# Kernel tuning notes

Measured on AMD Instinct MI355X. Metric: run time of the kernel, lower is better.

Reference implementation:

```python
import jax, jax.numpy as jnp
import numpy as np

B, L, H = 64, 512, 512  # batch_size, input_size (src len), hidden_size


def setup_inputs() -> dict:
    key = jax.random.key(0)
    ks = jax.random.split(key, 12)
    return {
        "encoder_outputs": jax.random.normal(ks[0], (B, L, H), dtype=jnp.float32),
        "attn_mask": jax.random.randint(ks[1], (B, L), 0, 2, dtype=jnp.int64),
        "hidden": jax.random.normal(ks[2], (B, H), dtype=jnp.float32),
        "coverage": jax.random.uniform(ks[3], (B, L), dtype=jnp.float32),
        # attnLin: Linear(H, H)
        "attn_w": jax.random.normal(ks[4], (H, H), dtype=jnp.float32) * 0.02,
        "attn_b": jax.random.normal(ks[5], (H,), dtype=jnp.float32) * 0.02,
        # decoderAttnLinear: Linear(H, H)
        "dec_w": jax.random.normal(ks[6], (H, H), dtype=jnp.float32) * 0.02,
        "dec_b": jax.random.normal(ks[7], (H,), dtype=jnp.float32) * 0.02,
        # cvgConv: Conv2d(L, L, kernel=(1, H), padding='same') -> weight [L, L, 1, H]
        "cvg_w": jax.random.normal(ks[8], (L, L, 1, H), dtype=jnp.float32) * 0.02,
        "cvg_b": jax.random.normal(ks[9], (L,), dtype=jnp.float32) * 0.02,
        # v parameter (trunc_normal in torch; plain normal is fine as a baseline)
        "v": jax.random.normal(ks[10], (B, H), dtype=jnp.float32),
    }


def reference(encoder_outputs, attn_mask, hidden, coverage,
              attn_w, attn_b, dec_w, dec_b, cvg_w, cvg_b, v):
    # Per-position linear loop in torch == one batched linear over [B, L, H].
    enc_feat = jnp.einsum('blh,oh->blo', encoder_outputs, attn_w) + attn_b  # [B,L,H]
    dec_feat = (hidden @ dec_w.T + dec_b)[:, None, :]                        # [B,1,H]
    # Coverage conv: input is [B, L(channels), 1, 1]; kernel (1, H) with 'same'
    # padding means only kernel column kw = (H-1)//2 ever overlaps the single
    # real (non-zero-padded) pixel, so the conv reduces exactly to a matmul
    # with that weight column plus bias. Same math, no wasted zero-multiplies.
    center = (H - 1) // 2
    w_eff = cvg_w[:, :, 0, center]                                           # [L_out, L_in]
    cov_feat = (coverage @ w_eff.T + cvg_b)[:, :, None]                      # [B,L,1]
    feats = jnp.tanh(enc_feat + dec_feat + cov_feat)                         # [B,L,H]
    scores = jnp.einsum('blh,bh->bl', feats, v)                              # [B,L]
    scores = jnp.where(attn_mask == 1, scores, -jnp.inf)
    attn_weights = jax.nn.softmax(scores, axis=1)                            # [B,L]
    new_coverage = coverage + attn_weights                                   # coverage += aw
    context_vector = jnp.einsum('bl,blh->bh', attn_weights, encoder_outputs) # [B,H]
    return context_vector, attn_weights, new_coverage
```

## Files before the change

kernel.cpp:

```cpp
#include <hip/hip_runtime.h>

#define B_ 64
#define L_ 512
#define H_ 512
#define CENTER 255

typedef float  f32x4  __attribute__((ext_vector_type(4)));
typedef _Float16 f16x8 __attribute__((ext_vector_type(8)));
typedef unsigned short u16x4 __attribute__((ext_vector_type(4)));
typedef unsigned short USH;


__device__ __forceinline__ float fast_tanh(float x) {
    float e = __expf(2.0f * x);
    return 1.0f - 2.0f * __builtin_amdgcn_rcpf(e + 1.0f);
}

__launch_bounds__(512)
__global__ void pre_kernel(const float* __restrict__ cvg_w, const float* __restrict__ cvg_b,
                           const float* __restrict__ coverage,
                           const float* __restrict__ aw, USH* __restrict__ bh16,
                           const float* __restrict__ hidden, const float* __restrict__ dec_w,
                           const float* __restrict__ dec_b,
                           float* __restrict__ dec_feat, float* __restrict__ cov_feat) {
    __shared__ float pool[34304];
    const int bid = blockIdx.x, t = threadIdx.x;
    if (bid < 512) {
        float* wl = pool;
        float* cs = pool + 512;
        const int i = bid;
        wl[t] = cvg_w[((size_t)(i * L_ + t)) * H_ + CENTER];
        #pragma unroll 8
        for (int c = 0; c < 64; ++c)
            cs[t * 65 + c] = coverage[c * L_ + t];
        __syncthreads();
        const int b = t >> 3, jg = t & 7;
        float sum = 0.f;
        #pragma unroll 8
        for (int jj = 0; jj < 64; ++jj) {
            int j = jg * 64 + ((jj + jg * 8) & 63);
            sum += cs[j * 65 + b] * wl[j];
        }
        sum += __shfl_xor(sum, 1, 64);
        sum += __shfl_xor(sum, 2, 64);
        sum += __shfl_xor(sum, 4, 64);
        if (jg == 0) cov_feat[b * L_ + i] = sum + cvg_b[i];
    } else if (bid < 640) {
        int i = (bid - 512) * 512 + t;
        float4 x = *(const float4*)&aw[(size_t)i * 4];
        float xs[4] = {x.x, x.y, x.z, x.w};
        u16x4 h;
        #pragma unroll
        for (int j = 0; j < 4; ++j)
            h[j] = __builtin_bit_cast(USH, (_Float16)xs[j]);
        *(u16x4*)&bh16[(size_t)i * 4] = h;
    } else {
        float* sbuf = pool;
        float* pr   = pool + 512;
        const int blk = bid - 640, b = blk >> 2, qq = blk & 3;
        const int ol = t & 127, part = t >> 7;
        sbuf[t] = hidden[b * H_ + t];
        __syncthreads();
        const float* row  = dec_w + (size_t)(qq * 128 + ol) * H_ + part * 128;
        const float* hseg = sbuf + part * 128;
        float d0 = 0.f, d1 = 0.f, d2 = 0.f, d3 = 0.f;
        #pragma unroll
        for (int k = 0; k < 128; k += 16) {
            float4 w0 = *(const float4*)&row[k];
            float4 w1 = *(const float4*)&row[k + 4];
            float4 w2 = *(const float4*)&row[k + 8];
            float4 w3 = *(const float4*)&row[k + 12];
            d0 += w0.x * hseg[k]      + w0.y * hseg[k + 1]  + w0.z * hseg[k + 2]  + w0.w * hseg[k + 3];
            d1 += w1.x * hseg[k + 4]  + w1.y * hseg[k + 5]  + w1.z * hseg[k + 6]  + w1.w * hseg[k + 7];
            d2 += w2.x * hseg[k + 8]  + w2.y * hseg[k + 9]  + w2.z * hseg[k + 10] + w2.w * hseg[k + 11];
            d3 += w3.x * hseg[k + 12] + w3.y * hseg[k + 13] + w3.z * hseg[k + 14] + w3.w * hseg[k + 15];
        }
        pr[t] = d0 + d1 + d2 + d3;
        __syncthreads();
        if (t < 128)
            dec_feat[b * H_ + qq * 128 + t] = pr[t] + pr[t + 128] + pr[t + 256] + pr[t + 384]
                                              + dec_b[qq * 128 + t];
    }
}

#define BM 128

#define STAGE_B(BUF, KS1)                                                                  \
    {                                                                                      \
        _Pragma("unroll")                                                                  \
        for (int it = 0; it < 2; ++it)                                                     \
            __builtin_amdgcn_global_load_lds(                                              \
                (const __attribute__((address_space(1))) void*)(bh16 + goffB[it] + (KS1) * 32), \
                (__attribute__((address_space(3))) void*)&Bsh[BUF][(wv * 2 + it) * 512],   \
                16, 0, 0);                                                                 \
    }

#define CVTWRITEA(BUF, A4)                                                                 \
    {                                                                                      \
        float axs[4] = {A4.x, A4.y, A4.z, A4.w};                                           \
        u16x4 hh;                                                                          \
        _Pragma("unroll")                                                                  \
        for (int j = 0; j < 4; ++j)                                                        \
            hh[j] = __builtin_bit_cast(USH, (_Float16)axs[j]);                             \
        *(u16x4*)&Ash[BUF][awoff] = hh;                                                    \
    }

__launch_bounds__(1024, 4)
__global__ void fused_score_mfma(const float* __restrict__ enc,
                                 const USH* __restrict__ bh16,
                                 const float* __restrict__ attn_b,
                                 const float* __restrict__ dec_feat,
                                 const float* __restrict__ cov_feat,
                                 const float* __restrict__ v,
                                 float* __restrict__ scores) {
    __shared__ USH Bsh[3][16384];
    __shared__ USH Ash[2][4096];

    const int t  = threadIdx.x;
    const int wv = t >> 6, ln = t & 63;
    const int wr = wv >> 3, wc = wv & 7;
    const int q  = ln >> 4, cl = ln & 15;
    const int m0 = blockIdx.x * BM;
    const int b  = blockIdx.x >> 2;

    int goffB[2];
    #pragma unroll
    for (int it = 0; it < 2; ++it) {
        int c   = wv * 2 + it;
        int srl = ln >> 3;
        int u   = (ln & 7) ^ (srl & 7);
        int n   = c * 16 + srl * 2 + (u >> 2);
        goffB[it] = n * 512 + (u & 3) * 8;
    }
    const int sA   = (((cl & 1) * 4 + q) ^ ((cl >> 1) & 7)) * 8;
    const int aoff = wr * 2048 + (cl >> 1) * 64 + sA;
    const int boff = wc * 2048 + (cl >> 1) * 64 + sA;

    const int arow = t >> 3, akoct = t & 7;
    const int asw  = ((arow & 1) * 4 + (akoct >> 1)) ^ ((arow >> 1) & 7);
    const int awoff = (arow >> 1) * 64 + asw * 8 + (akoct & 1) * 4;
    const float* agsrc = enc + (size_t)(m0 + arow) * H_ + akoct * 4;

    f32x4 acc[4][4];
    #pragma unroll
    for (int mf = 0; mf < 4; ++mf)
        #pragma unroll
        for (int nf = 0; nf < 4; ++nf) acc[mf][nf] = (f32x4){0.f, 0.f, 0.f, 0.f};

    float4 aP = *(const float4*)(agsrc + 32);
    float4 c0 = *(const float4*)agsrc;
    __builtin_amdgcn_sched_barrier(0);
    STAGE_B(0, 0);
    STAGE_B(1, 1);
    __builtin_amdgcn_sched_barrier(0);
    CVTWRITEA(0, c0);
    asm volatile("s_waitcnt lgkmcnt(0)" ::: "memory");
    asm volatile("s_waitcnt vmcnt(2)" ::: "memory");
    __builtin_amdgcn_sched_barrier(0);
    __builtin_amdgcn_s_barrier();

    #pragma unroll
    for (int ks = 0; ks < 16; ++ks) {
        const int curB = ks % 3;
        const int curA = ks & 1, nxtA = curA ^ 1;
        float4 aN;
        if (ks < 14) {
            STAGE_B((ks + 2) % 3, ks + 2);
            aN = *(const float4*)(agsrc + (ks + 2) * 32);
            __builtin_amdgcn_sched_barrier(0);
        }

        f16x8 ah[4];
        #pragma unroll
        for (int mf = 0; mf < 4; ++mf)
            ah[mf] = *(const f16x8*)&Ash[curA][aoff + mf * 512];
        __builtin_amdgcn_s_setprio(1);
        #pragma unroll
        for (int nf = 0; nf < 4; ++nf) {
            f16x8 bh = *(const f16x8*)&Bsh[curB][boff + nf * 512];
            #pragma unroll
            for (int mf = 0; mf < 4; ++mf)
                acc[mf][nf] = __builtin_amdgcn_mfma_f32_16x16x32_f16(ah[mf], bh, acc[mf][nf], 0, 0, 0);
        }
        __builtin_amdgcn_s_setprio(0);

        if (ks < 15) {
            CVTWRITEA(nxtA, aP);
            aP = aN;
            asm volatile("s_waitcnt lgkmcnt(0)" ::: "memory");
            if (ks < 14)
                asm volatile("s_waitcnt vmcnt(3)" ::: "memory");
            else
                asm volatile("s_waitcnt vmcnt(0)" ::: "memory");
            __builtin_amdgcn_sched_barrier(0);
            __builtin_amdgcn_s_barrier();
        }
    }
    __syncthreads();

    float (*scred)[BM] = (float (*)[BM])Ash;
    float addv[4], vvv[4];
    #pragma unroll
    for (int nf = 0; nf < 4; ++nf) {
        int n = wc * 64 + nf * 16 + cl;
        addv[nf] = attn_b[n] + dec_feat[b * H_ + n];
        vvv[nf]  = v[b * H_ + n];
    }
    #pragma unroll
    for (int mf = 0; mf < 4; ++mf) {
        #pragma unroll
        for (int reg = 0; reg < 4; ++reg) {
            int row = wr * 64 + mf * 16 + q * 4 + reg;
            float cf = cov_feat[m0 + row];
            float s = 0.f;
            #pragma unroll
            for (int nf = 0; nf < 4; ++nf)
                s += fast_tanh(acc[mf][nf][reg] + addv[nf] + cf) * vvv[nf];
            s += __shfl_xor(s, 1, 64);
            s += __shfl_xor(s, 2, 64);
            s += __shfl_xor(s, 4, 64);
            s += __shfl_xor(s, 8, 64);
            if (cl == 0) scred[wc][row] = s;
        }
    }
    __syncthreads();
    if (t < BM) {
        float s = 0.f;
        #pragma unroll
        for (int g = 0; g < 8; ++g) s += scred[g][t];
        scores[m0 + t] = s;
    }
}

__launch_bounds__(512)
__global__ void smctx_kernel(const float* __restrict__ scores, const int* __restrict__ mask,
                             const float* __restrict__ coverage, const float* __restrict__ enc,
                             float* __restrict__ out) {
    __shared__ float w[512];
    __shared__ float red[8];
    __shared__ float red2[8];
    __shared__ float cred[4][128];
    const int bid = blockIdx.x, b = bid >> 2, hc = bid & 3, t = threadIdx.x;
    const int idx = b * L_ + t;
    bool m = (mask[idx] == 1);
    float s = scores[idx];
    float val = m ? s : -INFINITY;

    float r = val;
    #pragma unroll
    for (int d = 1; d <= 32; d <<= 1) r = fmaxf(r, __shfl_xor(r, d, 64));
    if ((t & 63) == 0) red[t >> 6] = r;
    __syncthreads();
    float gmax = red[0];
    #pragma unroll
    for (int i = 1; i < 8; ++i) gmax = fmaxf(gmax, red[i]);

    float p = m ? __expf(s - gmax) : 0.f;
    float qq = p;
    #pragma unroll
    for (int d = 1; d <= 32; d <<= 1) qq += __shfl_xor(qq, d, 64);
    if ((t & 63) == 0) red2[t >> 6] = qq;
    __syncthreads();
    float tot = 0.f;
    #pragma unroll
    for (int i = 0; i < 8; ++i) tot += red2[i];

    float wt = p / tot;
    w[t] = wt;
    if (hc == 0) {
        out[B_ * H_ + idx] = wt;
        out[B_ * H_ + B_ * L_ + idx] = coverage[idx] + wt;
    }
    __syncthreads();

    const int ls = t >> 7, hb = t & 127;
    const float* ep = enc + (size_t)b * (L_ * H_) + hc * 128 + hb;
    float a0 = 0.f, a1 = 0.f, a2 = 0.f, a3 = 0.f;
    for (int l = ls; l < L_; l += 16) {
        a0 += w[l]      * ep[(size_t)l * H_];
        a1 += w[l + 4]  * ep[(size_t)(l + 4) * H_];
        a2 += w[l + 8]  * ep[(size_t)(l + 8) * H_];
        a3 += w[l + 12] * ep[(size_t)(l + 12) * H_];
    }
    cred[ls][hb] = a0 + a1 + a2 + a3;
    __syncthreads();
    if (t < 128)
        out[b * H_ + hc * 128 + t] = cred[0][t] + cred[1][t] + cred[2][t] + cred[3][t];
}

extern "C" void kernel_launch(void* const* d_in, const int* in_sizes, int n_in,
                              void* d_out, int out_size, void* d_ws, size_t ws_size,
                              hipStream_t stream) {
    const float* enc      = (const float*)d_in[0];
    const int*   mask     = (const int*)d_in[1];
    const float* hidden   = (const float*)d_in[2];
    const float* coverage = (const float*)d_in[3];
    const float* attn_w   = (const float*)d_in[4];
    const float* attn_b   = (const float*)d_in[5];
    const float* dec_w    = (const float*)d_in[6];
    const float* dec_b    = (const float*)d_in[7];
    const float* cvg_w    = (const float*)d_in[8];
    const float* cvg_b    = (const float*)d_in[9];
    const float* v        = (const float*)d_in[10];
    float* out = (float*)d_out;
    float* ws  = (float*)d_ws;
    float* scores   = ws;
    float* dec_feat = ws + 32768;
    float* cov_feat = ws + 65536;
    USH* bpk = (USH*)(ws + 360448);

    hipLaunchKernelGGL(pre_kernel,       dim3(896),  dim3(512),  0, stream,
                       cvg_w, cvg_b, coverage, attn_w, bpk, hidden, dec_w, dec_b,
                       dec_feat, cov_feat);
    hipLaunchKernelGGL(fused_score_mfma, dim3(256),  dim3(1024), 0, stream,
                       enc, bpk, attn_b, dec_feat, cov_feat, v, scores);
    hipLaunchKernelGGL(smctx_kernel,     dim3(256),  dim3(512),  0, stream,
                       scores, mask, coverage, enc, out);
}
```

Measured before the change: 70.07 us.

## Fuse softmax and context reduction into score kernel via cooperative grid sync

Merges the softmax/context kernel into the MFMA score kernel through a cooperative launch and a grid-wide sync. After the sync, each block recomputes the row softmax and accumulates the context over its own 128-row tile of encoder outputs, which that block just streamed and may still be in cache. Partial context sums are combined with atomicAdd into an output that is zeroed before the sync. This removes one kernel launch and possibly a second pass over the encoder from DRAM. The costs are a grid barrier, redundant softmax work in every block, and float atomics that make the summation order nondeterministic.

Measured after the change: 104.9 us. +49.7%, slower.

```diff
diff --git a/kernel.cpp b/kernel.cpp
--- a/kernel.cpp
+++ b/kernel.cpp
@@ -1,4 +1,7 @@
 #include <hip/hip_runtime.h>
+#include <hip/hip_cooperative_groups.h>
+
+namespace cg = cooperative_groups;
 
 #define B_ 64
 #define L_ 512
@@ -112,7 +115,10 @@
                                  const float* __restrict__ dec_feat,
                                  const float* __restrict__ cov_feat,
                                  const float* __restrict__ v,
-                                 float* __restrict__ scores) {
+                                 float* __restrict__ scores,
+                                 const int* __restrict__ mask,
+                                 const float* __restrict__ coverage,
+                                 float* __restrict__ out) {
     __shared__ USH Bsh[3][16384];
     __shared__ USH Ash[2][4096];
 
@@ -122,6 +128,7 @@
     const int q  = ln >> 4, cl = ln & 15;
     const int m0 = blockIdx.x * BM;
     const int b  = blockIdx.x >> 2;
+    const int lt = blockIdx.x & 3;
 
     int goffB[2];
     #pragma unroll
@@ -230,62 +237,66 @@
         for (int g = 0; g < 8; ++g) s += scred[g][t];
         scores[m0 + t] = s;
     }
-}
-
-__launch_bounds__(512)
-__global__ void smctx_kernel(const float* __restrict__ scores, const int* __restrict__ mask,
-                             const float* __restrict__ coverage, const float* __restrict__ enc,
-                             float* __restrict__ out) {
-    __shared__ float w[512];
-    __shared__ float red[8];
-    __shared__ float red2[8];
-    __shared__ float cred[4][128];
-    const int bid = blockIdx.x, b = bid >> 2, hc = bid & 3, t = threadIdx.x;
-    const int idx = b * L_ + t;
-    bool m = (mask[idx] == 1);
-    float s = scores[idx];
-    float val = m ? s : -INFINITY;
-
+
+    if (lt == 1 && t < 512) out[b * H_ + t] = 0.f;
+
+    cg::this_grid().sync();
+
+    float* wsm    = (float*)&Bsh[0][0];
+    float* red16  = wsm + 512;
+    float* red16b = wsm + 544;
+    float sv = 0.f; bool mk = false;
+    if (t < 512) { mk = (mask[b * L_ + t] == 1); sv = scores[b * L_ + t]; }
+    float val = (t < 512 && mk) ? sv : -INFINITY;
     float r = val;
     #pragma unroll
     for (int d = 1; d <= 32; d <<= 1) r = fmaxf(r, __shfl_xor(r, d, 64));
-    if ((t & 63) == 0) red[t >> 6] = r;
-    __syncthreads();
-    float gmax = red[0];
-    #pragma unroll
-    for (int i = 1; i < 8; ++i) gmax = fmaxf(gmax, red[i]);
-
-    float p = m ? __expf(s - gmax) : 0.f;
+    if (ln == 0) red16[wv] = r;
+    __syncthreads();
+    float gmax = red16[0];
+    #pragma unroll
+    for (int i = 1; i < 16; ++i) gmax = fmaxf(gmax, red16[i]);
+    float p = (t < 512 && mk) ? __expf(sv - gmax) : 0.f;
     float qq = p;
     #pragma unroll
     for (int d = 1; d <= 32; d <<= 1) qq += __shfl_xor(qq, d, 64);
-    if ((t & 63) == 0) red2[t >> 6] = qq;
+    if (ln == 0) red16b[wv] = qq;
     __syncthreads();
     float tot = 0.f;
     #pragma unroll
-    for (int i = 0; i < 8; ++i) tot += red2[i];
-
+    for (int i = 0; i < 16; ++i) tot += red16b[i];
     float wt = p / tot;
-    w[t] = wt;
-    if (hc == 0) {
-        out[B_ * H_ + idx] = wt;
-        out[B_ * H_ + B_ * L_ + idx] = coverage[idx] + wt;
-    }
-    __syncthreads();
-
-    const int ls = t >> 7, hb = t & 127;
-    const float* ep = enc + (size_t)b * (L_ * H_) + hc * 128 + hb;
-    float a0 = 0.f, a1 = 0.f, a2 = 0.f, a3 = 0.f;
-    for (int l = ls; l < L_; l += 16) {
-        a0 += w[l]      * ep[(size_t)l * H_];
-        a1 += w[l + 4]  * ep[(size_t)(l + 4) * H_];
-        a2 += w[l + 8]  * ep[(size_t)(l + 8) * H_];
-        a3 += w[l + 12] * ep[(size_t)(l + 12) * H_];
-    }
-    cred[ls][hb] = a0 + a1 + a2 + a3;
-    __syncthreads();
-    if (t < 128)
-        out[b * H_ + hc * 128 + t] = cred[0][t] + cred[1][t] + cred[2][t] + cred[3][t];
+    if (t < 512) {
+        wsm[t] = wt;
+        if (lt == 0) {
+            out[B_ * H_ + b * L_ + t] = wt;
+            out[B_ * H_ + B_ * L_ + b * L_ + t] = coverage[b * L_ + t] + wt;
+        }
+    }
+    __syncthreads();
+
+    {
+        const int h4 = t & 127, rg = t >> 7;
+        const float4* ebase = (const float4*)enc
+                              + ((size_t)(b * 512 + lt * 128 + rg * 16)) * 128 + h4;
+        const float* wloc = wsm + lt * 128 + rg * 16;
+        float4 a4 = {0.f, 0.f, 0.f, 0.f};
+        #pragma unroll
+        for (int k = 0; k < 16; ++k) {
+            float wl_ = wloc[k];
+            float4 e = ebase[(size_t)k * 128];
+            a4.x += wl_ * e.x; a4.y += wl_ * e.y; a4.z += wl_ * e.z; a4.w += wl_ * e.w;
+        }
+        ((float4*)Ash)[rg * 128 + h4] = a4;
+        __syncthreads();
+        if (t < 512) {
+            const float* Ar = (const float*)Ash;
+            float csum = 0.f;
+            #pragma unroll
+            for (int g = 0; g < 8; ++g) csum += Ar[g * 512 + t];
+            atomicAdd(&out[b * H_ + t], csum);
+        }
+    }
 }
 
 extern "C" void kernel_launch(void* const* d_in, const int* in_sizes, int n_in,
@@ -309,11 +320,13 @@
     float* cov_feat = ws + 65536;
     USH* bpk = (USH*)(ws + 360448);
 
-    hipLaunchKernelGGL(pre_kernel,       dim3(896),  dim3(512),  0, stream,
+    hipLaunchKernelGGL(pre_kernel, dim3(896), dim3(512), 0, stream,
                        cvg_w, cvg_b, coverage, attn_w, bpk, hidden, dec_w, dec_b,
                        dec_feat, cov_feat);
-    hipLaunchKernelGGL(fused_score_mfma, dim3(256),  dim3(1024), 0, stream,
-                       enc, bpk, attn_b, dec_feat, cov_feat, v, scores);
-    hipLaunchKernelGGL(smctx_kernel,     dim3(256),  dim3(512),  0, stream,
-                       scores, mask, coverage, enc, out);
+
+    void* kargs[] = {(void*)&enc, (void*)&bpk, (void*)&attn_b, (void*)&dec_feat,
+                     (void*)&cov_feat, (void*)&v, (void*)&scores, (void*)&mask,
+                     (void*)&coverage, (void*)&out};
+    hipLaunchCooperativeKernel((const void*)fused_score_mfma, dim3(256), dim3(1024),
+                               kargs, 0, stream);
 }
```
